# Performance work log

Hardware: AMD Instinct MI355X
Metric: run time of the kernel (lower is better)

## Reference

```python
import jax, jax.numpy as jnp
import numpy as np

N_NODES = 100000
N_EDGES = 1600000
NFEAT, NHID, NCLASS = 256, 128, 40


def setup_inputs() -> dict:
    key = jax.random.key(0)
    ks = jax.random.split(key, 10)
    x = jax.random.normal(ks[0], (N_NODES, NFEAT), dtype=jnp.float32)
    edge_row = jnp.sort(jax.random.randint(ks[1], (N_EDGES,), 0, N_NODES, dtype=jnp.int64))
    edge_col = jax.random.randint(ks[2], (N_EDGES,), 0, N_NODES, dtype=jnp.int64)
    edge_val = jax.random.uniform(ks[3], (N_EDGES,), dtype=jnp.float32)
    s = 0.05  # small init scale for numerical stability
    w1 = jax.random.normal(ks[4], (NFEAT, NHID), dtype=jnp.float32) * s
    b1 = jax.random.normal(ks[5], (NHID,), dtype=jnp.float32) * s
    w2 = jax.random.normal(ks[6], (NHID, NHID // 2), dtype=jnp.float32) * s
    b2 = jax.random.normal(ks[7], (NHID // 2,), dtype=jnp.float32) * s
    wl = jax.random.normal(ks[8], (NHID + NHID // 2, NCLASS), dtype=jnp.float32) * s
    bl = jax.random.normal(ks[9], (NCLASS,), dtype=jnp.float32) * s
    return {"x": x, "edge_row": edge_row, "edge_col": edge_col, "edge_val": edge_val,
            "w1": w1, "b1": b1, "w2": w2, "b2": b2, "wl": wl, "bl": bl}


def _gcn_layer(h, w, b, edge_row, edge_col, edge_val, n_nodes):
    # support = h @ W; out = spmm(adj, support) + b  (pygcn GraphConvolution)
    support = h @ w                                   # [N, d_out]
    msg = support[edge_col] * edge_val[:, None]       # gather src + edge weight, [E, d_out]
    agg = jax.ops.segment_sum(msg, edge_row, num_segments=n_nodes)  # scatter-add to dst
    return agg + b


def reference(x, edge_row, edge_col, edge_val, w1, b1, w2, b2, wl, bl):
    n = x.shape[0]
    x1 = jax.nn.relu(_gcn_layer(x, w1, b1, edge_row, edge_col, edge_val, n))
    # dropout is identity in eval mode
    x2 = jax.nn.relu(_gcn_layer(x1, w2, b2, edge_row, edge_col, edge_val, n))
    out = jnp.concatenate([x2, x1], axis=1) @ wl + bl
    return jax.nn.log_softmax(out, axis=-1)
```

## Files before the change

kernel.cpp:

```cpp
#include <hip/hip_runtime.h>
#include <math.h>

#define N_NODES 100000
#define N_EDGES 1600000
#define NFEAT   256
#define NHID    128
#define NHID2   64
#define NCLASS  40
#define NCLS_P  64

typedef __attribute__((ext_vector_type(8))) short bf16x8;
typedef __attribute__((ext_vector_type(4))) float f32x4;
typedef __attribute__((ext_vector_type(2))) float f32x2;

static __device__ inline unsigned short f2bf(float f) {
    union { float f; unsigned u; } v; v.f = f;
    unsigned r = v.u + 0x7FFF + ((v.u >> 16) & 1);
    return (unsigned short)(r >> 16);
}
static __device__ inline unsigned pkbf(float a, float b) {
    return (unsigned)f2bf(a) | ((unsigned)f2bf(b) << 16);
}
static __device__ inline float bfl(unsigned u) {
    union { unsigned u; float f; } v; v.u = u << 16; return v.f;
}
static __device__ inline float bfraw(unsigned u) {
    union { unsigned u; float f; } v; v.u = u; return v.f;
}

#define PREP_T0 (N_NODES + 1)
#define PREP_T1 (PREP_T0 + NHID * NFEAT)
#define PREP_T2 (PREP_T1 + NHID2 * NHID)
#define PREP_T3 (PREP_T2 + NCLS_P * 192)
#define PREP_T4 (PREP_T3 + N_EDGES)
__global__ void prep(const int* __restrict__ er, int* __restrict__ row_ptr,
                     const float* __restrict__ w1, unsigned short* __restrict__ w1t,
                     const float* __restrict__ w2, unsigned short* __restrict__ w2t,
                     const float* __restrict__ wl, unsigned short* __restrict__ wlt,
                     const int* __restrict__ ec, const float* __restrict__ ev,
                     uint2* __restrict__ meta) {
    int idx = blockIdx.x * blockDim.x + threadIdx.x;
    if (idx < PREP_T0) {
        int lo = 0, hi = N_EDGES;
        while (lo < hi) { int mid = (lo + hi) >> 1; if (er[mid] < idx) lo = mid + 1; else hi = mid; }
        row_ptr[idx] = lo;
    } else if (idx < PREP_T1) {
        int i = idx - PREP_T0;
        int n = i >> 8, k = i & 255;
        w1t[i] = f2bf(w1[k * NHID + n]);
    } else if (idx < PREP_T2) {
        int i = idx - PREP_T1;
        int n = i >> 7, k = i & 127;
        w2t[i] = f2bf(w2[k * NHID2 + n]);
    } else if (idx < PREP_T3) {
        int i = idx - PREP_T2;
        int n = i / 192, k = i - n * 192;
        wlt[i] = (n < NCLASS) ? f2bf(wl[k * NCLASS + n]) : (unsigned short)0;
    } else if (idx < PREP_T4) {
        int i = idx - PREP_T3;
        uint2 m; m.x = (unsigned)ec[i];
        union { float f; unsigned u; } v; v.f = ev[i];
        m.y = v.u;
        meta[i] = m;
    }
}

template <int BN, int ABF16, int CBF16>
__global__ __launch_bounds__(512) void gemm_bf16(const void* __restrict__ A,
                                                 const unsigned short* __restrict__ Bt,
                                                 void* __restrict__ C,
                                                 int M, int K, int lda) {
    const int BKP = 40;
    const int WC = (BN == 128) ? 4 : 2;
    const int WR = 8 / WC;
    const int MF = (128 / WR) / 16;
    const int NF = (BN / WC) / 16;
    __shared__ unsigned short As[2][128 * BKP];
    __shared__ unsigned short Bs[2][BN * BKP];

    int tid = threadIdx.x;
    int lane = tid & 63, wid = tid >> 6;
    int wr = wid / WC, wc = wid % WC;
    int row0 = blockIdx.x * 128;

    f32x4 acc[MF][NF];
    #pragma unroll
    for (int i = 0; i < MF; ++i)
        #pragma unroll
        for (int j = 0; j < NF; ++j) acc[i][j] = f32x4{0.f, 0.f, 0.f, 0.f};

    float4 arf[2]; uint4 arb; uint4 brg;

    auto LOAD = [&](int t) {
        int k0 = t * 32;
        if (ABF16) {
            const unsigned short* Ab = (const unsigned short*)A;
            int m = tid >> 2, k = (tid & 3) * 8;
            int row = row0 + m;
            arb = (row < M) ? *(const uint4*)(Ab + (size_t)row * lda + k0 + k)
                            : uint4{0u, 0u, 0u, 0u};
        } else {
            const float* Af = (const float*)A;
            #pragma unroll
            for (int i = 0; i < 2; ++i) {
                int s = tid + i * 512;
                int m = s >> 3, k = (s & 7) * 4;
                int row = row0 + m;
                arf[i] = (row < M) ? *(const float4*)(Af + (size_t)row * lda + k0 + k)
                                   : float4{0.f, 0.f, 0.f, 0.f};
            }
        }
        if (BN == 128 || tid < 256) {
            int n = tid >> 2, k = (tid & 3) * 8;
            brg = *(const uint4*)(Bt + (size_t)n * K + k0 + k);
        }
    };
    auto STORE = [&](int b) {
        if (ABF16) {
            int m = tid >> 2, k = (tid & 3) * 8;
            *(uint4*)&As[b][m * BKP + k] = arb;
        } else {
            #pragma unroll
            for (int i = 0; i < 2; ++i) {
                int s = tid + i * 512;
                int m = s >> 3, k = (s & 7) * 4;
                uint2 p; p.x = pkbf(arf[i].x, arf[i].y); p.y = pkbf(arf[i].z, arf[i].w);
                *(uint2*)&As[b][m * BKP + k] = p;
            }
        }
        if (BN == 128 || tid < 256) {
            int n = tid >> 2, k = (tid & 3) * 8;
            *(uint4*)&Bs[b][n * BKP + k] = brg;
        }
    };

    const int NT = K / 32;
    LOAD(0); STORE(0);
    __syncthreads();
    for (int t = 0; t < NT; ++t) {
        int cur = t & 1;
        if (t + 1 < NT) LOAD(t + 1);
        bf16x8 af[MF], bfr[NF];
        #pragma unroll
        for (int mi = 0; mi < MF; ++mi)
            af[mi] = *(const bf16x8*)&As[cur][(wr * (MF * 16) + mi * 16 + (lane & 15)) * BKP + (lane >> 4) * 8];
        #pragma unroll
        for (int ni = 0; ni < NF; ++ni)
            bfr[ni] = *(const bf16x8*)&Bs[cur][(wc * (NF * 16) + ni * 16 + (lane & 15)) * BKP + (lane >> 4) * 8];
        #pragma unroll
        for (int mi = 0; mi < MF; ++mi)
            #pragma unroll
            for (int ni = 0; ni < NF; ++ni)
                acc[mi][ni] = __builtin_amdgcn_mfma_f32_16x16x32_bf16(af[mi], bfr[ni], acc[mi][ni], 0, 0, 0);
        if (t + 1 < NT) {
            STORE(cur ^ 1);
            __syncthreads();
        }
    }

    #pragma unroll
    for (int mi = 0; mi < MF; ++mi) {
        int rbase = row0 + wr * (MF * 16) + mi * 16 + ((lane >> 4) << 2);
        #pragma unroll
        for (int ni = 0; ni < NF; ++ni) {
            int col = wc * (NF * 16) + ni * 16 + (lane & 15);
            #pragma unroll
            for (int r = 0; r < 4; ++r) {
                int row = rbase + r;
                if (row < M) {
                    if (CBF16) ((unsigned short*)C)[(size_t)row * BN + col] = f2bf(acc[mi][ni][r]);
                    else       ((float*)C)[(size_t)row * BN + col] = acc[mi][ni][r];
                }
            }
        }
    }
}

template <int D>
__global__ __launch_bounds__(256) void spmm_bias_relu(const unsigned short* __restrict__ sup,
                                                      const int* __restrict__ row_ptr,
                                                      const uint2* __restrict__ meta,
                                                      const float* __restrict__ bias,
                                                      unsigned short* __restrict__ out,
                                                      int out_stride, int n_nodes) {
    const int EPG   = (D == 128) ? 2 : 4;
    const int JSTEP = 8 * EPG;
    const int SHIFT = (D == 128) ? 8 : 7;

    __shared__ uint2 mlds[4][64];

    int wave = threadIdx.x >> 6;
    int lane = threadIdx.x & 63;
    int node = blockIdx.x * 4 + wave;
    if (node >= n_nodes) return;

    int sub = (D == 128) ? (lane >> 5) : (lane >> 4);
    int l   = (D == 128) ? (lane & 31) : (lane & 15);

    int e0 = row_ptr[node];
    int cnt = row_ptr[node + 1] - e0;
    const char* base = (const char*)sup;
    unsigned loff = (unsigned)(l << 3);

    f32x2 a0 = {0.f, 0.f}, a1 = {0.f, 0.f};

    for (int o = 0; o < cnt; o += 64) {
        int rem = min(64, cnt - o);
        uint2 m;
        if (lane < rem) m = meta[e0 + o + lane];
        else { m.x = 0u; m.y = 0u; }
        mlds[wave][lane] = m;

        for (int j = 0; j < rem; j += JSTEP) {
            uint2 g[8]; float vv[8];
            #pragma unroll
            for (int t = 0; t < 8; ++t) {
                uint2 cm = mlds[wave][j + t * EPG + sub];
                unsigned voff = (cm.x << SHIFT) + loff;
                g[t] = *(const uint2*)(base + voff);
                union { unsigned u; float f; } c; c.u = cm.y;
                vv[t] = c.f;
            }
            #pragma unroll
            for (int t = 0; t < 8; ++t) {
                f32x2 v2 = {vv[t], vv[t]};
                f32x2 f0 = {bfl(g[t].x), bfraw(g[t].x)};
                f32x2 f1 = {bfl(g[t].y), bfraw(g[t].y)};
                a0 += v2 * f0;
                a1 += v2 * f1;
            }
        }
    }

    a0.x += __shfl_xor(a0.x, 32); a0.y += __shfl_xor(a0.y, 32);
    a1.x += __shfl_xor(a1.x, 32); a1.y += __shfl_xor(a1.y, 32);
    if (D == 64) {
        a0.x += __shfl_xor(a0.x, 16); a0.y += __shfl_xor(a0.y, 16);
        a1.x += __shfl_xor(a1.x, 16); a1.y += __shfl_xor(a1.y, 16);
    }

    if (lane < ((D == 128) ? 32 : 16)) {
        float4 bv = *(const float4*)(bias + 4 * l);
        float r0 = a0.x + bv.x, r1 = a0.y + bv.y;
        float r2 = a1.x + bv.z, r3 = a1.y + bv.w;
        r0 = r0 > 0.f ? r0 : 0.f; r1 = r1 > 0.f ? r1 : 0.f;
        r2 = r2 > 0.f ? r2 : 0.f; r3 = r3 > 0.f ? r3 : 0.f;
        uint2 pk; pk.x = pkbf(r0, r1); pk.y = pkbf(r2, r3);
        *(uint2*)(out + (size_t)node * out_stride + 4 * l) = pk;
    }
}

__global__ __launch_bounds__(512) void head_fused(const unsigned short* __restrict__ A,
                                                  const unsigned short* __restrict__ Bt,
                                                  const float* __restrict__ bl,
                                                  float* __restrict__ out, int M) {
    const int BKP = 40;
    const int MF = 2, NF = 2;
    __shared__ unsigned short As[2][128 * BKP];
    __shared__ unsigned short Bs[2][64 * BKP];
    __shared__ float L[128][65];
    __shared__ float bls[NCLASS];

    int tid = threadIdx.x;
    int lane = tid & 63, wid = tid >> 6;
    int wr = wid >> 1, wc = wid & 1;
    int row0 = blockIdx.x * 128;
    if (tid < NCLASS) bls[tid] = bl[tid];

    f32x4 acc[MF][NF];
    #pragma unroll
    for (int i = 0; i < MF; ++i)
        #pragma unroll
        for (int j = 0; j < NF; ++j) acc[i][j] = f32x4{0.f, 0.f, 0.f, 0.f};

    uint4 arb, brg;
    auto LOAD = [&](int t) {
        int k0 = t * 32;
        int m = tid >> 2, k = (tid & 3) * 8;
        int row = row0 + m;
        arb = (row < M) ? *(const uint4*)(A + (size_t)row * 192 + k0 + k)
                        : uint4{0u, 0u, 0u, 0u};
        if (tid < 256) brg = *(const uint4*)(Bt + (size_t)m * 192 + k0 + k);
    };
    auto STORE = [&](int b) {
        int m = tid >> 2, k = (tid & 3) * 8;
        *(uint4*)&As[b][m * BKP + k] = arb;
        if (tid < 256) *(uint4*)&Bs[b][m * BKP + k] = brg;
    };

    const int NT = 6;
    LOAD(0); STORE(0);
    __syncthreads();
    for (int t = 0; t < NT; ++t) {
        int cur = t & 1;
        if (t + 1 < NT) LOAD(t + 1);
        bf16x8 af[MF], bfr[NF];
        #pragma unroll
        for (int mi = 0; mi < MF; ++mi)
            af[mi] = *(const bf16x8*)&As[cur][(wr * 32 + mi * 16 + (lane & 15)) * BKP + (lane >> 4) * 8];
        #pragma unroll
        for (int ni = 0; ni < NF; ++ni)
            bfr[ni] = *(const bf16x8*)&Bs[cur][(wc * 32 + ni * 16 + (lane & 15)) * BKP + (lane >> 4) * 8];
        #pragma unroll
        for (int mi = 0; mi < MF; ++mi)
            #pragma unroll
            for (int ni = 0; ni < NF; ++ni)
                acc[mi][ni] = __builtin_amdgcn_mfma_f32_16x16x32_bf16(af[mi], bfr[ni], acc[mi][ni], 0, 0, 0);
        if (t + 1 < NT) {
            STORE(cur ^ 1);
            __syncthreads();
        }
    }

    #pragma unroll
    for (int mi = 0; mi < MF; ++mi) {
        int rt = wr * 32 + mi * 16 + ((lane >> 4) << 2);
        #pragma unroll
        for (int ni = 0; ni < NF; ++ni) {
            int ct = wc * 32 + ni * 16 + (lane & 15);
            #pragma unroll
            for (int r = 0; r < 4; ++r) L[rt + r][ct] = acc[mi][ni][r];
        }
    }
    __syncthreads();

    {
        int r = tid >> 2, h = tid & 3;
        int row = row0 + r;
        if (row < M) {
            float vals[10];
            float m = -1e30f;
            #pragma unroll
            for (int c = 0; c < 10; ++c) {
                float tv = L[r][h * 10 + c] + bls[h * 10 + c];
                vals[c] = tv;
                m = fmaxf(m, tv);
            }
            m = fmaxf(m, __shfl_xor(m, 1));
            m = fmaxf(m, __shfl_xor(m, 2));
            float s = 0.f;
            #pragma unroll
            for (int c = 0; c < 10; ++c) s += __expf(vals[c] - m);
            s += __shfl_xor(s, 1);
            s += __shfl_xor(s, 2);
            float lg = __logf(s);
            float* o = out + (size_t)row * NCLASS + h * 10;
            #pragma unroll
            for (int c = 0; c < 10; ++c) o[c] = vals[c] - m - lg;
        }
    }
}

extern "C" void kernel_launch(void* const* d_in, const int* in_sizes, int n_in,
                              void* d_out, int out_size, void* d_ws, size_t ws_size,
                              hipStream_t stream) {
    const float* x        = (const float*)d_in[0];
    const int*   edge_row = (const int*)d_in[1];
    const int*   edge_col = (const int*)d_in[2];
    const float* edge_val = (const float*)d_in[3];
    const float* w1       = (const float*)d_in[4];
    const float* b1       = (const float*)d_in[5];
    const float* w2       = (const float*)d_in[6];
    const float* b2       = (const float*)d_in[7];
    const float* wl       = (const float*)d_in[8];
    const float* bl       = (const float*)d_in[9];
    float* out = (float*)d_out;
    (void)in_sizes; (void)n_in; (void)out_size; (void)ws_size;

    char* ws = (char*)d_ws;
    size_t off = 0;
    int* row_ptr = (int*)(ws + off);
    off += (((size_t)(N_NODES + 1) * sizeof(int)) + 255) & ~(size_t)255;
    unsigned short* x_cat = (unsigned short*)(ws + off);
    off += (size_t)N_NODES * 192 * sizeof(short);
    unsigned short* sup = (unsigned short*)(ws + off);
    off += (size_t)N_NODES * NHID * sizeof(short);
    uint2* meta = (uint2*)(ws + off);   off += (size_t)N_EDGES * sizeof(uint2);
    unsigned short* w1t = (unsigned short*)(ws + off); off += (size_t)NHID * NFEAT * sizeof(short);
    unsigned short* w2t = (unsigned short*)(ws + off); off += (size_t)NHID2 * NHID * sizeof(short);
    unsigned short* wlt = (unsigned short*)(ws + off); off += (size_t)NCLS_P * 192 * sizeof(short);

    unsigned short* x1 = x_cat + NHID2;
    unsigned short* x2 = x_cat;

    prep<<<(PREP_T4 + 255) / 256, 256, 0, stream>>>(edge_row, row_ptr, w1, w1t, w2, w2t, wl, wlt,
                                                    edge_col, edge_val, meta);

    int mblocks = (N_NODES + 127) / 128;

    gemm_bf16<NHID, 0, 1><<<dim3(mblocks, 1), 512, 0, stream>>>(x, w1t, sup, N_NODES, NFEAT, NFEAT);
    spmm_bias_relu<NHID><<<(N_NODES + 3) / 4, 256, 0, stream>>>(
        sup, row_ptr, meta, b1, x1, 192, N_NODES);

    gemm_bf16<NHID2, 1, 1><<<dim3(mblocks, 1), 512, 0, stream>>>(x1, w2t, sup, N_NODES, NHID, 192);
    spmm_bias_relu<NHID2><<<(N_NODES + 3) / 4, 256, 0, stream>>>(
        sup, row_ptr, meta, b2, x2, 192, N_NODES);

    head_fused<<<dim3(mblocks, 1), 512, 0, stream>>>(x_cat, wlt, bl, out, N_NODES);
}
```

Baseline: 167.1 us.

## Gather layer-1 support in FP8 and deepen GEMM prefetch pipeline

Layer 1's bf16 support matrix is now converted to FP8 (e4m3) by a separate kernel, and the first SpMM gathers 128-byte FP8 rows instead of 256-byte bf16 rows, halving the bytes moved in the gather. The GEMM now takes K as a template parameter, fully unrolls its k-loop and keeps two register prefetch stages so loads are issued further ahead. The extra conversion pass costs a read and write of the support matrix. FP8 quantization loses precision that could push errors past tolerance.

New measurement: 163.4 us. 2.2% less time.

```diff
diff --git a/kernel.cpp b/kernel.cpp
--- a/kernel.cpp
+++ b/kernel.cpp
@@ -26,6 +26,49 @@
 }
 static __device__ inline float bfraw(unsigned u) {
     union { unsigned u; float f; } v; v.u = u; return v.f;
+}
+
+#if __has_builtin(__builtin_amdgcn_cvt_pk_fp8_f32) && __has_builtin(__builtin_amdgcn_cvt_pk_f32_fp8)
+#define FP8_HW 1
+#else
+#define FP8_HW 0
+static __device__ inline unsigned f2fp8_sw(float f) {
+    union { float f; unsigned u; } v; v.f = f;
+    unsigned s = (v.u >> 24) & 0x80u;
+    int e = (int)((v.u >> 23) & 0xFF) - 120;
+    unsigned m = v.u & 0x7FFFFFu;
+    if (e < 1) return s;
+    unsigned keep = m >> 20, rest = m & 0xFFFFFu;
+    keep += (rest > 0x80000u) || (rest == 0x80000u && (keep & 1));
+    if (keep == 8) { keep = 0; ++e; }
+    if (e > 15) { e = 15; keep = 6; }
+    return s | ((unsigned)e << 3) | keep;
+}
+static __device__ inline float fp8f_sw(unsigned b) {
+    unsigned e = (b >> 3) & 0xF;
+    union { unsigned u; float f; } v;
+    v.u = ((b & 0x80u) << 24) | ((e + 120) << 23) | ((b & 7u) << 20);
+    return e ? v.f : 0.f;
+}
+#endif
+
+static __device__ inline unsigned pack4_fp8(float a, float b, float c, float d) {
+#if FP8_HW
+    int r = __builtin_amdgcn_cvt_pk_fp8_f32(a, b, 0, false);
+    r = __builtin_amdgcn_cvt_pk_fp8_f32(c, d, r, true);
+    return (unsigned)r;
+#else
+    return f2fp8_sw(a) | (f2fp8_sw(b) << 8) | (f2fp8_sw(c) << 16) | (f2fp8_sw(d) << 24);
+#endif
+}
+static __device__ inline void unpack4_fp8(unsigned g, f32x2& lo, f32x2& hi) {
+#if FP8_HW
+    lo = __builtin_amdgcn_cvt_pk_f32_fp8((int)g, false);
+    hi = __builtin_amdgcn_cvt_pk_f32_fp8((int)g, true);
+#else
+    lo.x = fp8f_sw(g & 0xFF); lo.y = fp8f_sw((g >> 8) & 0xFF);
+    hi.x = fp8f_sw((g >> 16) & 0xFF); hi.y = fp8f_sw(g >> 24);
+#endif
 }
 
 #define PREP_T0 (N_NODES + 1)
@@ -65,12 +108,24 @@
     }
 }
 
-template <int BN, int ABF16, int CBF16>
+__global__ __launch_bounds__(256) void conv_fp8(const uint4* __restrict__ sup16,
+                                                uint2* __restrict__ sup8, int nw) {
+    int i = blockIdx.x * blockDim.x + threadIdx.x;
+    if (i >= nw) return;
+    uint4 s = sup16[i];
+    uint2 r;
+    r.x = pack4_fp8(bfl(s.x), bfraw(s.x), bfl(s.y), bfraw(s.y));
+    r.y = pack4_fp8(bfl(s.z), bfraw(s.z), bfl(s.w), bfraw(s.w));
+    sup8[i] = r;
+}
+
+template <int BN, int K, int ABF16, int CBF16>
 __global__ __launch_bounds__(512) void gemm_bf16(const void* __restrict__ A,
                                                  const unsigned short* __restrict__ Bt,
                                                  void* __restrict__ C,
-                                                 int M, int K, int lda) {
+                                                 int M, int lda) {
     const int BKP = 40;
+    const int NT = K / 32;
     const int WC = (BN == 128) ? 4 : 2;
     const int WR = 8 / WC;
     const int MF = (128 / WR) / 16;
@@ -89,16 +144,16 @@
         #pragma unroll
         for (int j = 0; j < NF; ++j) acc[i][j] = f32x4{0.f, 0.f, 0.f, 0.f};
 
-    float4 arf[2]; uint4 arb; uint4 brg;
-
-    auto LOAD = [&](int t) {
+    float4 arf[2][2]; uint4 arb[2]; uint4 brg[2];
+
+    auto LOAD = [&](int t, int b) {
         int k0 = t * 32;
         if (ABF16) {
             const unsigned short* Ab = (const unsigned short*)A;
             int m = tid >> 2, k = (tid & 3) * 8;
             int row = row0 + m;
-            arb = (row < M) ? *(const uint4*)(Ab + (size_t)row * lda + k0 + k)
-                            : uint4{0u, 0u, 0u, 0u};
+            arb[b] = (row < M) ? *(const uint4*)(Ab + (size_t)row * lda + k0 + k)
+                               : uint4{0u, 0u, 0u, 0u};
         } else {
             const float* Af = (const float*)A;
             #pragma unroll
@@ -106,40 +161,42 @@
                 int s = tid + i * 512;
                 int m = s >> 3, k = (s & 7) * 4;
                 int row = row0 + m;
-                arf[i] = (row < M) ? *(const float4*)(Af + (size_t)row * lda + k0 + k)
-                                   : float4{0.f, 0.f, 0.f, 0.f};
+                arf[b][i] = (row < M) ? *(const float4*)(Af + (size_t)row * lda + k0 + k)
+                                      : float4{0.f, 0.f, 0.f, 0.f};
             }
         }
         if (BN == 128 || tid < 256) {
             int n = tid >> 2, k = (tid & 3) * 8;
-            brg = *(const uint4*)(Bt + (size_t)n * K + k0 + k);
+            brg[b] = *(const uint4*)(Bt + (size_t)n * K + k0 + k);
         }
     };
-    auto STORE = [&](int b) {
+    auto STORE = [&](int t, int b) {
+        int buf = t & 1;
         if (ABF16) {
             int m = tid >> 2, k = (tid & 3) * 8;
-            *(uint4*)&As[b][m * BKP + k] = arb;
+            *(uint4*)&As[buf][m * BKP + k] = arb[b];
         } else {
             #pragma unroll
             for (int i = 0; i < 2; ++i) {
                 int s = tid + i * 512;
                 int m = s >> 3, k = (s & 7) * 4;
-                uint2 p; p.x = pkbf(arf[i].x, arf[i].y); p.y = pkbf(arf[i].z, arf[i].w);
-                *(uint2*)&As[b][m * BKP + k] = p;
+                uint2 p; p.x = pkbf(arf[b][i].x, arf[b][i].y); p.y = pkbf(arf[b][i].z, arf[b][i].w);
+                *(uint2*)&As[buf][m * BKP + k] = p;
             }
         }
         if (BN == 128 || tid < 256) {
             int n = tid >> 2, k = (tid & 3) * 8;
-            *(uint4*)&Bs[b][n * BKP + k] = brg;
+            *(uint4*)&Bs[buf][n * BKP + k] = brg[b];
         }
     };
 
-    const int NT = K / 32;
-    LOAD(0); STORE(0);
+    LOAD(0, 0); STORE(0, 0); LOAD(1, 1);
+    if (NT > 2) LOAD(2, 0);
     __syncthreads();
+
+    #pragma unroll
     for (int t = 0; t < NT; ++t) {
         int cur = t & 1;
-        if (t + 1 < NT) LOAD(t + 1);
         bf16x8 af[MF], bfr[NF];
         #pragma unroll
         for (int mi = 0; mi < MF; ++mi)
@@ -153,7 +210,8 @@
             for (int ni = 0; ni < NF; ++ni)
                 acc[mi][ni] = __builtin_amdgcn_mfma_f32_16x16x32_bf16(af[mi], bfr[ni], acc[mi][ni], 0, 0, 0);
         if (t + 1 < NT) {
-            STORE(cur ^ 1);
+            STORE(t + 1, (t + 1) & 1);
+            if (t + 3 < NT) LOAD(t + 3, (t + 1) & 1);
             __syncthreads();
         }
     }
@@ -176,17 +234,12 @@
     }
 }
 
-template <int D>
-__global__ __launch_bounds__(256) void spmm_bias_relu(const unsigned short* __restrict__ sup,
-                                                      const int* __restrict__ row_ptr,
-                                                      const uint2* __restrict__ meta,
-                                                      const float* __restrict__ bias,
-                                                      unsigned short* __restrict__ out,
-                                                      int out_stride, int n_nodes) {
-    const int EPG   = (D == 128) ? 2 : 4;
-    const int JSTEP = 8 * EPG;
-    const int SHIFT = (D == 128) ? 8 : 7;
-
+__global__ __launch_bounds__(256) void spmm_fp8(const unsigned char* __restrict__ sup8,
+                                                const int* __restrict__ row_ptr,
+                                                const uint2* __restrict__ meta,
+                                                const float* __restrict__ bias,
+                                                unsigned short* __restrict__ out,
+                                                int out_stride, int n_nodes) {
     __shared__ uint2 mlds[4][64];
 
     int wave = threadIdx.x >> 6;
@@ -194,13 +247,10 @@
     int node = blockIdx.x * 4 + wave;
     if (node >= n_nodes) return;
 
-    int sub = (D == 128) ? (lane >> 5) : (lane >> 4);
-    int l   = (D == 128) ? (lane & 31) : (lane & 15);
-
+    int sub = lane >> 5, l = lane & 31;
     int e0 = row_ptr[node];
     int cnt = row_ptr[node + 1] - e0;
-    const char* base = (const char*)sup;
-    unsigned loff = (unsigned)(l << 3);
+    unsigned loff = (unsigned)(l << 2);
 
     f32x2 a0 = {0.f, 0.f}, a1 = {0.f, 0.f};
 
@@ -211,12 +261,74 @@
         else { m.x = 0u; m.y = 0u; }
         mlds[wave][lane] = m;
 
-        for (int j = 0; j < rem; j += JSTEP) {
+        for (int j = 0; j < rem; j += 16) {
+            unsigned g[8]; float vv[8];
+            #pragma unroll
+            for (int t = 0; t < 8; ++t) {
+                uint2 cm = mlds[wave][j + 2 * t + sub];
+                g[t] = *(const unsigned*)(sup8 + (((size_t)cm.x) << 7) + loff);
+                union { unsigned u; float f; } c; c.u = cm.y;
+                vv[t] = c.f;
+            }
+            #pragma unroll
+            for (int t = 0; t < 8; ++t) {
+                f32x2 lo, hi;
+                unpack4_fp8(g[t], lo, hi);
+                f32x2 v2 = {vv[t], vv[t]};
+                a0 += v2 * lo;
+                a1 += v2 * hi;
+            }
+        }
+    }
+
+    a0.x += __shfl_xor(a0.x, 32); a0.y += __shfl_xor(a0.y, 32);
+    a1.x += __shfl_xor(a1.x, 32); a1.y += __shfl_xor(a1.y, 32);
+
+    if (lane < 32) {
+        float4 bv = *(const float4*)(bias + 4 * l);
+        float r0 = a0.x + bv.x, r1 = a0.y + bv.y;
+        float r2 = a1.x + bv.z, r3 = a1.y + bv.w;
+        r0 = r0 > 0.f ? r0 : 0.f; r1 = r1 > 0.f ? r1 : 0.f;
+        r2 = r2 > 0.f ? r2 : 0.f; r3 = r3 > 0.f ? r3 : 0.f;
+        uint2 pk; pk.x = pkbf(r0, r1); pk.y = pkbf(r2, r3);
+        *(uint2*)(out + (size_t)node * out_stride + 4 * l) = pk;
+    }
+}
+
+__global__ __launch_bounds__(256) void spmm_bf16_64(const unsigned short* __restrict__ sup,
+                                                    const int* __restrict__ row_ptr,
+                                                    const uint2* __restrict__ meta,
+                                                    const float* __restrict__ bias,
+                                                    unsigned short* __restrict__ out,
+                                                    int out_stride, int n_nodes) {
+    __shared__ uint2 mlds[4][64];
+
+    int wave = threadIdx.x >> 6;
+    int lane = threadIdx.x & 63;
+    int node = blockIdx.x * 4 + wave;
+    if (node >= n_nodes) return;
+
+    int sub = lane >> 4, l = lane & 15;
+    int e0 = row_ptr[node];
+    int cnt = row_ptr[node + 1] - e0;
+    const char* base = (const char*)sup;
+    unsigned loff = (unsigned)(l << 3);
+
+    f32x2 a0 = {0.f, 0.f}, a1 = {0.f, 0.f};
+
+    for (int o = 0; o < cnt; o += 64) {
+        int rem = min(64, cnt - o);
+        uint2 m;
+        if (lane < rem) m = meta[e0 + o + lane];
+        else { m.x = 0u; m.y = 0u; }
+        mlds[wave][lane] = m;
+
+        for (int j = 0; j < rem; j += 32) {
             uint2 g[8]; float vv[8];
             #pragma unroll
             for (int t = 0; t < 8; ++t) {
-                uint2 cm = mlds[wave][j + t * EPG + sub];
-                unsigned voff = (cm.x << SHIFT) + loff;
+                uint2 cm = mlds[wave][j + 4 * t + sub];
+                unsigned voff = (cm.x << 7) + loff;
                 g[t] = *(const uint2*)(base + voff);
                 union { unsigned u; float f; } c; c.u = cm.y;
                 vv[t] = c.f;
@@ -234,12 +346,10 @@
 
     a0.x += __shfl_xor(a0.x, 32); a0.y += __shfl_xor(a0.y, 32);
     a1.x += __shfl_xor(a1.x, 32); a1.y += __shfl_xor(a1.y, 32);
-    if (D == 64) {
-        a0.x += __shfl_xor(a0.x, 16); a0.y += __shfl_xor(a0.y, 16);
-        a1.x += __shfl_xor(a1.x, 16); a1.y += __shfl_xor(a1.y, 16);
-    }
-
-    if (lane < ((D == 128) ? 32 : 16)) {
+    a0.x += __shfl_xor(a0.x, 16); a0.y += __shfl_xor(a0.y, 16);
+    a1.x += __shfl_xor(a1.x, 16); a1.y += __shfl_xor(a1.y, 16);
+
+    if (lane < 16) {
         float4 bv = *(const float4*)(bias + 4 * l);
         float r0 = a0.x + bv.x, r1 = a0.y + bv.y;
         float r2 = a1.x + bv.z, r3 = a1.y + bv.w;
@@ -291,6 +401,7 @@
     const int NT = 6;
     LOAD(0); STORE(0);
     __syncthreads();
+    #pragma unroll
     for (int t = 0; t < NT; ++t) {
         int cur = t & 1;
         if (t + 1 < NT) LOAD(t + 1);
@@ -375,6 +486,8 @@
     off += (size_t)N_NODES * 192 * sizeof(short);
     unsigned short* sup = (unsigned short*)(ws + off);
     off += (size_t)N_NODES * NHID * sizeof(short);
+    unsigned char* sup8 = (unsigned char*)(ws + off);
+    off += (size_t)N_NODES * NHID;
     uint2* meta = (uint2*)(ws + off);   off += (size_t)N_EDGES * sizeof(uint2);
     unsigned short* w1t = (unsigned short*)(ws + off); off += (size_t)NHID * NFEAT * sizeof(short);
     unsigned short* w2t = (unsigned short*)(ws + off); off += (size_t)NHID2 * NHID * sizeof(short);
@@ -388,13 +501,13 @@
 
     int mblocks = (N_NODES + 127) / 128;
 
-    gemm_bf16<NHID, 0, 1><<<dim3(mblocks, 1), 512, 0, stream>>>(x, w1t, sup, N_NODES, NFEAT, NFEAT);
-    spmm_bias_relu<NHID><<<(N_NODES + 3) / 4, 256, 0, stream>>>(
-        sup, row_ptr, meta, b1, x1, 192, N_NODES);
-
-    gemm_bf16<NHID2, 1, 1><<<dim3(mblocks, 1), 512, 0, stream>>>(x1, w2t, sup, N_NODES, NHID, 192);
-    spmm_bias_relu<NHID2><<<(N_NODES + 3) / 4, 256, 0, stream>>>(
-        sup, row_ptr, meta, b2, x2, 192, N_NODES);
+    gemm_bf16<NHID, NFEAT, 0, 1><<<dim3(mblocks, 1), 512, 0, stream>>>(x, w1t, sup, N_NODES, NFEAT);
+    conv_fp8<<<(N_NODES * NHID / 8 + 255) / 256, 256, 0, stream>>>((const uint4*)sup, (uint2*)sup8,
+                                                                   N_NODES * NHID / 8);
+    spmm_fp8<<<(N_NODES + 3) / 4, 256, 0, stream>>>(sup8, row_ptr, meta, b1, x1, 192, N_NODES);
+
+    gemm_bf16<NHID2, NHID, 1, 1><<<dim3(mblocks, 1), 512, 0, stream>>>(x1, w2t, sup, N_NODES, 192);
+    spmm_bf16_64<<<(N_NODES + 3) / 4, 256, 0, stream>>>(sup, row_ptr, meta, b2, x2, 192, N_NODES);
 
     head_fused<<<dim3(mblocks, 1), 512, 0, stream>>>(x_cat, wlt, bl, out, N_NODES);
 }
```
